# Kernel optimization log

Hardware: AMD Instinct MI355X
Metric: run time of the kernel (lower is better)

The kernel has to match this reference:

```python
import jax, jax.numpy as jnp
import numpy as np

DIM = 2048
HEADS = 16
HEAD_DIM = DIM // HEADS
B, S = 2, 2048


def setup_inputs() -> dict:
    key = jax.random.key(0)
    k1, k2, k3 = jax.random.split(key, 3)
    x = jax.random.normal(k1, (B, S, DIM), dtype=jnp.float32)
    # causal mask (True = keep), realistic production usage of masked_fill(mask==0,...)
    mask = jnp.tril(jnp.ones((S, S), dtype=bool))
    scale = 1.0 / np.sqrt(DIM)
    W_qkv = jax.random.normal(k2, (DIM, 3 * DIM), dtype=jnp.float32) * scale
    b_qkv = jnp.zeros((3 * DIM,), dtype=jnp.float32)
    W_out = jax.random.normal(k3, (DIM, DIM), dtype=jnp.float32) * scale
    b_out = jnp.zeros((DIM,), dtype=jnp.float32)
    return {"x": x, "mask": mask, "W_qkv": W_qkv, "b_qkv": b_qkv,
            "W_out": W_out, "b_out": b_out}


def reference(x, mask, W_qkv, b_qkv, W_out, b_out):
    b, s, d = x.shape
    # fused QKV projection: [b,s,3d]
    qkv = jnp.einsum('bsd,de->bse', x, W_qkv) + b_qkv
    # [b, s, h, 3*hd] -> [b, h, s, 3*hd] -> chunk into q,k,v
    qkv = qkv.reshape(b, s, HEADS, 3 * HEAD_DIM).transpose(0, 2, 1, 3)
    q, k, v = jnp.split(qkv, 3, axis=-1)  # each [b,h,s,hd]
    scores = jnp.einsum('bhqd,bhkd->bhqk', q, k) / np.sqrt(HEAD_DIM)
    scores = jnp.where(mask, scores, jnp.float32(-1e9))
    attn = jax.nn.softmax(scores, axis=-1)
    # dropout_rate = 0.0 (eval) -> identity
    out = jnp.einsum('bhqk,bhkd->bhqd', attn, v)  # [b,h,s,hd]
    out = out.transpose(0, 2, 1, 3).reshape(b, s, d)
    return jnp.einsum('bsd,de->bse', out, W_out) + b_out
```

## Files before the change

kernel.cpp:

```cpp
#include <hip/hip_runtime.h>
#include <hip/hip_bf16.h>

#define SEQ   2048
#define DIMSZ 2048
#define NHEAD 16
#define HD    128
#define KDIM  2048

typedef __attribute__((ext_vector_type(8))) short bf16x8;
typedef __attribute__((ext_vector_type(4))) float f32x4;
typedef __attribute__((ext_vector_type(4))) short short4v;
typedef __attribute__((ext_vector_type(4))) float float4v;

__device__ __forceinline__ short f2bf(float f) {
    union { __hip_bfloat16 h; short s; } u;
    u.h = __float2bfloat16(f);
    return u.s;
}

__device__ __forceinline__ void gload_lds16(const void* g, void* l) {
    __builtin_amdgcn_global_load_lds(
        (const __attribute__((address_space(1))) void*)g,
        (__attribute__((address_space(3))) void*)l, 16, 0, 0);
}

__global__ __launch_bounds__(256) void cvt_bf16(const float* __restrict__ in,
                                                short* __restrict__ out) {
    int i = (blockIdx.x * 256 + threadIdx.x) * 4;
    float4v v = *reinterpret_cast<const float4v*>(in + i);
    short4v o;
    o[0] = f2bf(v[0]); o[1] = f2bf(v[1]); o[2] = f2bf(v[2]); o[3] = f2bf(v[3]);
    *reinterpret_cast<short4v*>(out + i) = o;
}

__global__ __launch_bounds__(256) void transpose_cvt(const float* __restrict__ in,
                                                     short* __restrict__ out,
                                                     int R, int C) {
    __shared__ float tile[32][33];
    int c0 = blockIdx.x * 32, r0 = blockIdx.y * 32;
    int tx = threadIdx.x, ty = threadIdx.y;
#pragma unroll
    for (int i = 0; i < 32; i += 8)
        tile[ty + i][tx] = in[(long)(r0 + ty + i) * C + c0 + tx];
    __syncthreads();
#pragma unroll
    for (int i = 0; i < 32; i += 8)
        out[(long)(c0 + ty + i) * R + r0 + tx] = f2bf(tile[tx][ty + i]);
}

template <int MODE>
__global__ __launch_bounds__(256) void gemm_bt(const short* __restrict__ A,
                                               const short* __restrict__ Bt,
                                               const float* __restrict__ bias,
                                               float* __restrict__ outf,
                                               short* __restrict__ q_buf,
                                               short* __restrict__ k_buf,
                                               short* __restrict__ vt_buf) {
    __shared__ short Alds[128 * 64];
    __shared__ short Blds[128 * 64];
    const int tid = threadIdx.x;
    const int wave = tid >> 6, lane = tid & 63;
    const int lr = lane & 15, lg = lane >> 4;
    const int m0 = blockIdx.y * 128, n0 = blockIdx.x * 128;
    const int wr = (wave >> 1) * 64, wc = (wave & 1) * 64;
    const short* Ab = A + (long)m0 * KDIM;
    const short* Bb = Bt + (long)n0 * KDIM;
    const int srow = tid >> 3;
    const int sch = (tid & 7) * 8;

    f32x4 acc[4][4] = {};

    for (int kt = 0; kt < KDIM; kt += 64) {
#pragma unroll
        for (int i = 0; i < 4; ++i) {
            gload_lds16(Ab + (long)(i * 32 + srow) * KDIM + kt + sch,
                        &Alds[(i * 256 + wave * 64) * 8]);
            gload_lds16(Bb + (long)(i * 32 + srow) * KDIM + kt + sch,
                        &Blds[(i * 256 + wave * 64) * 8]);
        }
        __syncthreads();
#pragma unroll
        for (int kk = 0; kk < 2; ++kk) {
            bf16x8 af[4], bfr[4];
#pragma unroll
            for (int mi = 0; mi < 4; ++mi)
                af[mi] = *reinterpret_cast<const bf16x8*>(
                    &Alds[(wr + mi * 16 + lr) * 64 + kk * 32 + lg * 8]);
#pragma unroll
            for (int ni = 0; ni < 4; ++ni)
                bfr[ni] = *reinterpret_cast<const bf16x8*>(
                    &Blds[(wc + ni * 16 + lr) * 64 + kk * 32 + lg * 8]);
#pragma unroll
            for (int mi = 0; mi < 4; ++mi)
#pragma unroll
                for (int ni = 0; ni < 4; ++ni)
                    acc[mi][ni] = __builtin_amdgcn_mfma_f32_16x16x32_bf16(
                        af[mi], bfr[ni], acc[mi][ni], 0, 0, 0);
        }
        __syncthreads();
    }

#pragma unroll
    for (int mi = 0; mi < 4; ++mi) {
#pragma unroll
        for (int ni = 0; ni < 4; ++ni) {
            int col = n0 + wc + ni * 16 + lr;
            float bv = bias[col];
#pragma unroll
            for (int j = 0; j < 4; ++j) {
                int row = m0 + wr + mi * 16 + lg * 4 + j;
                float v = acc[mi][ni][j] + bv;
                if (MODE == 0) {
                    int h = col / (3 * HD);
                    int jj = col - h * (3 * HD);
                    int b = row >> 11, s = row & 2047;
                    int bh = b * NHEAD + h;
                    short sv = f2bf(v);
                    if (jj < HD)
                        q_buf[(bh * SEQ + s) * HD + jj] = sv;
                    else if (jj < 2 * HD)
                        k_buf[(bh * SEQ + s) * HD + (jj - HD)] = sv;
                    else
                        vt_buf[(bh * HD + (jj - 2 * HD)) * SEQ + s] = sv;
                } else {
                    outf[(long)row * DIMSZ + col] = v;
                }
            }
        }
    }
}

__global__ __launch_bounds__(256, 2) void attn_kernel(const short* __restrict__ q_buf,
                                                      const short* __restrict__ k_buf,
                                                      const short* __restrict__ vt_buf,
                                                      short* __restrict__ ao) {
    __shared__ __align__(16) short Klds[2][64 * 128];
    __shared__ __align__(16) short Vlds[2][128 * 64];
    __shared__ __align__(16) short Plds[4][32 * 64];
    const int tid = threadIdx.x;
    const int wave = tid >> 6, lane = tid & 63;
    const int lr = lane & 15, lg = lane >> 4;
    const int bx = blockIdx.x;
    const int qt = 15 - (bx >> 5);
    const int bh = bx & 31;
    const int b = bh >> 4, h = bh & 15;
    const int qbase = qt * 128 + wave * 32;
    const float scale = 0.08838834764831845f;

    bf16x8 qf[2][4];
    {
        const short* qrow = q_buf + ((long)(bh * SEQ + qbase + lr)) * HD;
#pragma unroll
        for (int mi = 0; mi < 2; ++mi)
#pragma unroll
            for (int c = 0; c < 4; ++c)
                qf[mi][c] = *reinterpret_cast<const bf16x8*>(
                    qrow + mi * 16 * HD + c * 32 + lg * 8);
    }
    asm volatile("s_waitcnt vmcnt(0)" ::: "memory");

    const char* kbase = (const char*)(k_buf + (long)bh * SEQ * HD);
    const char* vbase = (const char*)(vt_buf + (long)bh * HD * SEQ);
    const int krow_l = wave * 4 + (lane >> 4);
    const int kcol_l = ((lane & 15) * 16) ^ ((krow_l & 7) << 4);
    const int vrow_l = wave * 8 + (lane >> 3);
    const int vcol_l = ((lane & 7) * 16) ^ ((vrow_l & 7) << 4);

    const int nt = 2 * (qt + 1);
    auto stage = [&](int bufi, int t) {
        const char* ks = kbase + (long)t * 16384 + (long)krow_l * 256 + kcol_l;
        const char* vs = vbase + (long)t * 128 + (long)vrow_l * (SEQ * 2) + vcol_l;
        short* kd = &Klds[bufi][wave * 512];
        short* vd = &Vlds[bufi][wave * 512];
#pragma unroll
        for (int i = 0; i < 4; ++i) {
            gload_lds16(ks + i * 4096, kd + i * 2048);
            gload_lds16(vs + (long)i * 32 * SEQ * 2, vd + i * 2048);
        }
    };

    f32x4 o_acc[2][8] = {};
    float mrow[2][4], lrow[2][4];
#pragma unroll
    for (int mi = 0; mi < 2; ++mi)
#pragma unroll
        for (int j = 0; j < 4; ++j) { mrow[mi][j] = -1e30f; lrow[mi][j] = 0.f; }
    short* pw = &Plds[wave][0];

    stage(0, 0);
    for (int t = 0; t < nt; ++t) {
        const int cur = t & 1;
        if (t + 1 < nt) {
            stage(cur ^ 1, t + 1);
            asm volatile("s_waitcnt vmcnt(8)" ::: "memory");
        } else {
            asm volatile("s_waitcnt vmcnt(0)" ::: "memory");
        }
        __builtin_amdgcn_s_barrier();
        __builtin_amdgcn_sched_barrier(0);

        const int kv0 = t * 64;
        if (kv0 <= qbase + 31) {
            f32x4 sc[2][4] = {};
            const short* kl = &Klds[cur][0];
#pragma unroll
            for (int c = 0; c < 4; ++c) {
                bf16x8 kf[4];
#pragma unroll
                for (int ni = 0; ni < 4; ++ni)
                    kf[ni] = *reinterpret_cast<const bf16x8*>(
                        kl + (((ni * 16 + lr) * 256 +
                               ((c * 64 + lg * 16) ^ ((lr & 7) << 4))) >> 1));
#pragma unroll
                for (int mi = 0; mi < 2; ++mi)
#pragma unroll
                    for (int ni = 0; ni < 4; ++ni)
                        sc[mi][ni] = __builtin_amdgcn_mfma_f32_16x16x32_bf16(
                            qf[mi][c], kf[ni], sc[mi][ni], 0, 0, 0);
            }
            const bool full = (kv0 + 63) <= qbase;
            float pv[2][4][4], pm[2][4];
#pragma unroll
            for (int mi = 0; mi < 2; ++mi)
#pragma unroll
                for (int j = 0; j < 4; ++j) {
                    float mx = -3e38f;
#pragma unroll
                    for (int ni = 0; ni < 4; ++ni) {
                        float v = sc[mi][ni][j] * scale;
                        if (!full) {
                            int qg = qbase + mi * 16 + lg * 4 + j;
                            if (kv0 + ni * 16 + lr > qg) v = -1e9f;
                        }
                        pv[mi][ni][j] = v;
                        mx = fmaxf(mx, v);
                    }
                    pm[mi][j] = mx;
                }
#pragma unroll
            for (int m = 1; m < 16; m <<= 1)
#pragma unroll
                for (int mi = 0; mi < 2; ++mi)
#pragma unroll
                    for (int j = 0; j < 4; ++j)
                        pm[mi][j] = fmaxf(pm[mi][j], __shfl_xor(pm[mi][j], m, 64));
            float alpha[2][4], psum[2][4];
#pragma unroll
            for (int mi = 0; mi < 2; ++mi)
#pragma unroll
                for (int j = 0; j < 4; ++j) {
                    float mn = fmaxf(mrow[mi][j], pm[mi][j]);
                    alpha[mi][j] = __expf(mrow[mi][j] - mn);
                    mrow[mi][j] = mn;
                    psum[mi][j] = 0.f;
                }
#pragma unroll
            for (int mi = 0; mi < 2; ++mi)
#pragma unroll
                for (int ni = 0; ni < 4; ++ni)
#pragma unroll
                    for (int j = 0; j < 4; ++j) {
                        float p = __expf(pv[mi][ni][j] - mrow[mi][j]);
                        pv[mi][ni][j] = p;
                        psum[mi][j] += p;
                    }
#pragma unroll
            for (int m = 1; m < 16; m <<= 1)
#pragma unroll
                for (int mi = 0; mi < 2; ++mi)
#pragma unroll
                    for (int j = 0; j < 4; ++j)
                        psum[mi][j] += __shfl_xor(psum[mi][j], m, 64);
#pragma unroll
            for (int mi = 0; mi < 2; ++mi)
#pragma unroll
                for (int j = 0; j < 4; ++j)
                    lrow[mi][j] = lrow[mi][j] * alpha[mi][j] + psum[mi][j];
#pragma unroll
            for (int mi = 0; mi < 2; ++mi)
#pragma unroll
                for (int n = 0; n < 8; ++n)
#pragma unroll
                    for (int j = 0; j < 4; ++j)
                        o_acc[mi][n][j] *= alpha[mi][j];
#pragma unroll
            for (int mi = 0; mi < 2; ++mi)
#pragma unroll
                for (int ni = 0; ni < 4; ++ni)
#pragma unroll
                    for (int j = 0; j < 4; ++j) {
                        int row = mi * 16 + lg * 4 + j;
                        int cb = (ni * 32 + lr * 2) ^ ((row & 7) << 4);
                        pw[(row * 128 + cb) >> 1] = f2bf(pv[mi][ni][j]);
                    }
            const short* vl = &Vlds[cur][0];
#pragma unroll
            for (int kc = 0; kc < 2; ++kc) {
                bf16x8 pa[2];
#pragma unroll
                for (int mi = 0; mi < 2; ++mi)
                    pa[mi] = *reinterpret_cast<const bf16x8*>(
                        pw + (((mi * 16 + lr) * 128 +
                               ((kc * 64 + lg * 16) ^ ((lr & 7) << 4))) >> 1));
#pragma unroll
                for (int n = 0; n < 8; ++n) {
                    bf16x8 vf = *reinterpret_cast<const bf16x8*>(
                        vl + (((n * 16 + lr) * 128 +
                               ((kc * 64 + lg * 16) ^ ((lr & 7) << 4))) >> 1));
#pragma unroll
                    for (int mi = 0; mi < 2; ++mi)
                        o_acc[mi][n] = __builtin_amdgcn_mfma_f32_16x16x32_bf16(
                            pa[mi], vf, o_acc[mi][n], 0, 0, 0);
                }
            }
        }
        __builtin_amdgcn_s_barrier();
    }

    float inv[2][4];
#pragma unroll
    for (int mi = 0; mi < 2; ++mi)
#pragma unroll
        for (int j = 0; j < 4; ++j) inv[mi][j] = 1.0f / lrow[mi][j];
    short* aor = ao + ((long)(b * SEQ + qbase) * DIMSZ + h * HD);
#pragma unroll
    for (int mi = 0; mi < 2; ++mi)
#pragma unroll
        for (int n = 0; n < 8; ++n)
#pragma unroll
            for (int j = 0; j < 4; ++j)
                aor[(mi * 16 + lg * 4 + j) * DIMSZ + n * 16 + lr] =
                    f2bf(o_acc[mi][n][j] * inv[mi][j]);
}

extern "C" void kernel_launch(void* const* d_in, const int* in_sizes, int n_in,
                              void* d_out, int out_size, void* d_ws, size_t ws_size,
                              hipStream_t stream) {
    const float* x     = (const float*)d_in[0];
    const float* W_qkv = (const float*)d_in[2];
    const float* b_qkv = (const float*)d_in[3];
    const float* W_out = (const float*)d_in[4];
    const float* b_out = (const float*)d_in[5];
    float* out = (float*)d_out;

    char* ws = (char*)d_ws;
    short* x_bf   = (short*)ws;
    short* wqkv_t = (short*)(ws + (size_t)16 * 1048576);
    short* wout_t = (short*)(ws + (size_t)40 * 1048576);
    short* q_buf  = (short*)(ws + (size_t)48 * 1048576);
    short* k_buf  = (short*)(ws + (size_t)64 * 1048576);
    short* vt_buf = (short*)(ws + (size_t)80 * 1048576);
    short* ao     = x_bf;

    cvt_bf16<<<8192, 256, 0, stream>>>(x, x_bf);
    transpose_cvt<<<dim3(192, 64), dim3(32, 8), 0, stream>>>(W_qkv, wqkv_t, 2048, 6144);
    transpose_cvt<<<dim3(64, 64), dim3(32, 8), 0, stream>>>(W_out, wout_t, 2048, 2048);
    gemm_bt<0><<<dim3(48, 32), 256, 0, stream>>>(x_bf, wqkv_t, b_qkv, nullptr,
                                                 q_buf, k_buf, vt_buf);
    attn_kernel<<<512, 256, 0, stream>>>(q_buf, k_buf, vt_buf, ao);
    gemm_bt<1><<<dim3(16, 32), 256, 0, stream>>>(ao, wout_t, b_out, out,
                                                 nullptr, nullptr, nullptr);
}
```

Baseline: 339.9 us.

## Replace GEMM with 256x256 8-wave double-buffered pipelined kernel with LDS swizzle

New measurement: 352.3 us. 3.6% more time.

```diff
diff --git a/kernel.cpp b/kernel.cpp
--- a/kernel.cpp
+++ b/kernel.cpp
@@ -49,81 +49,191 @@
 }
 
 template <int MODE>
-__global__ __launch_bounds__(256) void gemm_bt(const short* __restrict__ A,
-                                               const short* __restrict__ Bt,
-                                               const float* __restrict__ bias,
-                                               float* __restrict__ outf,
-                                               short* __restrict__ q_buf,
-                                               short* __restrict__ k_buf,
-                                               short* __restrict__ vt_buf) {
-    __shared__ short Alds[128 * 64];
-    __shared__ short Blds[128 * 64];
+__global__ __launch_bounds__(512, 2) void gemm8p(const short* __restrict__ A,
+                                                 const short* __restrict__ Bt,
+                                                 const float* __restrict__ bias,
+                                                 float* __restrict__ outf,
+                                                 short* __restrict__ q_buf,
+                                                 short* __restrict__ k_buf,
+                                                 short* __restrict__ vt_buf,
+                                                 int ntx) {
+    __shared__ __align__(16) short Alds[2][256 * 64];
+    __shared__ __align__(16) short Blds[2][256 * 64];
     const int tid = threadIdx.x;
-    const int wave = tid >> 6, lane = tid & 63;
-    const int lr = lane & 15, lg = lane >> 4;
-    const int m0 = blockIdx.y * 128, n0 = blockIdx.x * 128;
-    const int wr = (wave >> 1) * 64, wc = (wave & 1) * 64;
-    const short* Ab = A + (long)m0 * KDIM;
-    const short* Bb = Bt + (long)n0 * KDIM;
-    const int srow = tid >> 3;
-    const int sch = (tid & 7) * 8;
-
-    f32x4 acc[4][4] = {};
-
-    for (int kt = 0; kt < KDIM; kt += 64) {
-#pragma unroll
-        for (int i = 0; i < 4; ++i) {
-            gload_lds16(Ab + (long)(i * 32 + srow) * KDIM + kt + sch,
-                        &Alds[(i * 256 + wave * 64) * 8]);
-            gload_lds16(Bb + (long)(i * 32 + srow) * KDIM + kt + sch,
-                        &Blds[(i * 256 + wave * 64) * 8]);
-        }
-        __syncthreads();
-#pragma unroll
-        for (int kk = 0; kk < 2; ++kk) {
-            bf16x8 af[4], bfr[4];
+    const int wv = tid >> 6, ln = tid & 63;
+    const int lr = ln & 15, lg = ln >> 4;
+    const int wr = wv >> 2, wc = wv & 3;
+    const int q8 = gridDim.x >> 3;
+    const int id = blockIdx.x;
+    const int swz = (id & 7) * q8 + (id >> 3);
+    const int m0 = (swz / ntx) * 256, n0 = (swz % ntx) * 256;
+
+    const int r_l = wv * 8 + (ln >> 3);
+    const int g8 = ((ln & 7) ^ ((ln >> 3) & 7)) << 3;
+
+    auto stA = [&](int bufi, int half, int T) {
+#pragma unroll
+        for (int i = 0; i < 2; ++i)
+            gload_lds16(A + (long)(m0 + half * 128 + i * 64 + r_l) * KDIM + T * 64 + g8,
+                        &Alds[bufi][half * 8192 + i * 4096 + wv * 512]);
+    };
+    auto stB = [&](int bufi, int half, int T) {
+#pragma unroll
+        for (int i = 0; i < 2; ++i)
+            gload_lds16(Bt + (long)(n0 + half * 128 + i * 64 + r_l) * KDIM + T * 64 + g8,
+                        &Blds[bufi][half * 8192 + i * 4096 + wv * 512]);
+    };
+
+    f32x4 acc[4][4][2] = {};
+
+    stA(0, 0, 0); stB(0, 0, 0); stA(0, 1, 0); stB(0, 1, 0);
+    stA(1, 0, 1); stB(1, 0, 1);
+    asm volatile("s_waitcnt vmcnt(4)" ::: "memory");
+    __builtin_amdgcn_s_barrier();
+    __builtin_amdgcn_sched_barrier(0);
+
+    const int NT = KDIM / 64;
+    int cur = 0;
+    for (int T = 0; T < NT; ++T, cur ^= 1) {
+        const short* Al = &Alds[cur][0];
+        const short* Bl = &Blds[cur][0];
+        auto rdA = [&](int r, int kk) {
+            return *reinterpret_cast<const bf16x8*>(
+                &Al[r * 64 + (((kk * 4 + lg) ^ (r & 7)) << 3)]);
+        };
+        auto rdB = [&](int r, int kk) {
+            return *reinterpret_cast<const bf16x8*>(
+                &Bl[r * 64 + (((kk * 4 + lg) ^ (r & 7)) << 3)]);
+        };
+        bf16x8 af[4][2], bf[2][2];
+
+#pragma unroll
+        for (int mi = 0; mi < 4; ++mi) {
+            af[mi][0] = rdA(wr * 64 + mi * 16 + lr, 0);
+            af[mi][1] = rdA(wr * 64 + mi * 16 + lr, 1);
+        }
+#pragma unroll
+        for (int ni = 0; ni < 2; ++ni) {
+            bf[ni][0] = rdB(wc * 32 + ni * 16 + lr, 0);
+            bf[ni][1] = rdB(wc * 32 + ni * 16 + lr, 1);
+        }
+        if (T + 1 < NT) stA(cur ^ 1, 1, T + 1);
+        __builtin_amdgcn_s_barrier();
+        __builtin_amdgcn_sched_barrier(0);
+        __builtin_amdgcn_s_setprio(1);
+#pragma unroll
+        for (int kk = 0; kk < 2; ++kk)
 #pragma unroll
             for (int mi = 0; mi < 4; ++mi)
-                af[mi] = *reinterpret_cast<const bf16x8*>(
-                    &Alds[(wr + mi * 16 + lr) * 64 + kk * 32 + lg * 8]);
-#pragma unroll
-            for (int ni = 0; ni < 4; ++ni)
-                bfr[ni] = *reinterpret_cast<const bf16x8*>(
-                    &Blds[(wc + ni * 16 + lr) * 64 + kk * 32 + lg * 8]);
+#pragma unroll
+                for (int ni = 0; ni < 2; ++ni)
+                    acc[0][mi][ni] = __builtin_amdgcn_mfma_f32_16x16x32_bf16(
+                        af[mi][kk], bf[ni][kk], acc[0][mi][ni], 0, 0, 0);
+        __builtin_amdgcn_s_setprio(0);
+        __builtin_amdgcn_s_barrier();
+        __builtin_amdgcn_sched_barrier(0);
+
+#pragma unroll
+        for (int ni = 0; ni < 2; ++ni) {
+            bf[ni][0] = rdB(128 + wc * 32 + ni * 16 + lr, 0);
+            bf[ni][1] = rdB(128 + wc * 32 + ni * 16 + lr, 1);
+        }
+        if (T + 1 < NT) stB(cur ^ 1, 1, T + 1);
+        __builtin_amdgcn_s_barrier();
+        __builtin_amdgcn_sched_barrier(0);
+        __builtin_amdgcn_s_setprio(1);
+#pragma unroll
+        for (int kk = 0; kk < 2; ++kk)
 #pragma unroll
             for (int mi = 0; mi < 4; ++mi)
 #pragma unroll
-                for (int ni = 0; ni < 4; ++ni)
-                    acc[mi][ni] = __builtin_amdgcn_mfma_f32_16x16x32_bf16(
-                        af[mi], bfr[ni], acc[mi][ni], 0, 0, 0);
-        }
-        __syncthreads();
+                for (int ni = 0; ni < 2; ++ni)
+                    acc[1][mi][ni] = __builtin_amdgcn_mfma_f32_16x16x32_bf16(
+                        af[mi][kk], bf[ni][kk], acc[1][mi][ni], 0, 0, 0);
+        __builtin_amdgcn_s_setprio(0);
+        __builtin_amdgcn_s_barrier();
+        __builtin_amdgcn_sched_barrier(0);
+
+#pragma unroll
+        for (int mi = 0; mi < 4; ++mi) {
+            af[mi][0] = rdA(128 + wr * 64 + mi * 16 + lr, 0);
+            af[mi][1] = rdA(128 + wr * 64 + mi * 16 + lr, 1);
+        }
+#pragma unroll
+        for (int ni = 0; ni < 2; ++ni) {
+            bf[ni][0] = rdB(wc * 32 + ni * 16 + lr, 0);
+            bf[ni][1] = rdB(wc * 32 + ni * 16 + lr, 1);
+        }
+        if (T + 2 < NT) stA(cur, 0, T + 2);
+        __builtin_amdgcn_s_barrier();
+        __builtin_amdgcn_sched_barrier(0);
+        __builtin_amdgcn_s_setprio(1);
+#pragma unroll
+        for (int kk = 0; kk < 2; ++kk)
+#pragma unroll
+            for (int mi = 0; mi < 4; ++mi)
+#pragma unroll
+                for (int ni = 0; ni < 2; ++ni)
+                    acc[2][mi][ni] = __builtin_amdgcn_mfma_f32_16x16x32_bf16(
+                        af[mi][kk], bf[ni][kk], acc[2][mi][ni], 0, 0, 0);
+        __builtin_amdgcn_s_setprio(0);
+        __builtin_amdgcn_s_barrier();
+        __builtin_amdgcn_sched_barrier(0);
+
+#pragma unroll
+        for (int ni = 0; ni < 2; ++ni) {
+            bf[ni][0] = rdB(128 + wc * 32 + ni * 16 + lr, 0);
+            bf[ni][1] = rdB(128 + wc * 32 + ni * 16 + lr, 1);
+        }
+        if (T + 2 < NT) stB(cur, 0, T + 2);
+        __builtin_amdgcn_s_barrier();
+        __builtin_amdgcn_sched_barrier(0);
+        __builtin_amdgcn_s_setprio(1);
+#pragma unroll
+        for (int kk = 0; kk < 2; ++kk)
+#pragma unroll
+            for (int mi = 0; mi < 4; ++mi)
+#pragma unroll
+                for (int ni = 0; ni < 2; ++ni)
+                    acc[3][mi][ni] = __builtin_amdgcn_mfma_f32_16x16x32_bf16(
+                        af[mi][kk], bf[ni][kk], acc[3][mi][ni], 0, 0, 0);
+        __builtin_amdgcn_s_setprio(0);
+        if (T + 2 < NT)
+            asm volatile("s_waitcnt vmcnt(4)" ::: "memory");
+        else if (T + 1 < NT)
+            asm volatile("s_waitcnt vmcnt(0)" ::: "memory");
+        __builtin_amdgcn_s_barrier();
+        __builtin_amdgcn_sched_barrier(0);
     }
 
 #pragma unroll
-    for (int mi = 0; mi < 4; ++mi) {
-#pragma unroll
-        for (int ni = 0; ni < 4; ++ni) {
-            int col = n0 + wc + ni * 16 + lr;
-            float bv = bias[col];
-#pragma unroll
-            for (int j = 0; j < 4; ++j) {
-                int row = m0 + wr + mi * 16 + lg * 4 + j;
-                float v = acc[mi][ni][j] + bv;
-                if (MODE == 0) {
-                    int h = col / (3 * HD);
-                    int jj = col - h * (3 * HD);
-                    int b = row >> 11, s = row & 2047;
-                    int bh = b * NHEAD + h;
-                    short sv = f2bf(v);
-                    if (jj < HD)
-                        q_buf[(bh * SEQ + s) * HD + jj] = sv;
-                    else if (jj < 2 * HD)
-                        k_buf[(bh * SEQ + s) * HD + (jj - HD)] = sv;
-                    else
-                        vt_buf[(bh * HD + (jj - 2 * HD)) * SEQ + s] = sv;
-                } else {
-                    outf[(long)row * DIMSZ + col] = v;
+    for (int q = 0; q < 4; ++q) {
+        const int mh = q >> 1, nh = q & 1;
+#pragma unroll
+        for (int mi = 0; mi < 4; ++mi) {
+#pragma unroll
+            for (int ni = 0; ni < 2; ++ni) {
+                int col = n0 + nh * 128 + wc * 32 + ni * 16 + lr;
+                float bv = bias[col];
+#pragma unroll
+                for (int j = 0; j < 4; ++j) {
+                    int row = m0 + mh * 128 + wr * 64 + mi * 16 + lg * 4 + j;
+                    float v = acc[q][mi][ni][j] + bv;
+                    if (MODE == 0) {
+                        int h = col / (3 * HD);
+                        int jj = col - h * (3 * HD);
+                        int b = row >> 11, s = row & 2047;
+                        int bh = b * NHEAD + h;
+                        short sv = f2bf(v);
+                        if (jj < HD)
+                            q_buf[(bh * SEQ + s) * HD + jj] = sv;
+                        else if (jj < 2 * HD)
+                            k_buf[(bh * SEQ + s) * HD + (jj - HD)] = sv;
+                        else
+                            vt_buf[(bh * HD + (jj - 2 * HD)) * SEQ + s] = sv;
+                    } else {
+                        outf[(long)row * DIMSZ + col] = v;
+                    }
                 }
             }
         }
@@ -355,9 +465,9 @@
     cvt_bf16<<<8192, 256, 0, stream>>>(x, x_bf);
     transpose_cvt<<<dim3(192, 64), dim3(32, 8), 0, stream>>>(W_qkv, wqkv_t, 2048, 6144);
     transpose_cvt<<<dim3(64, 64), dim3(32, 8), 0, stream>>>(W_out, wout_t, 2048, 2048);
-    gemm_bt<0><<<dim3(48, 32), 256, 0, stream>>>(x_bf, wqkv_t, b_qkv, nullptr,
-                                                 q_buf, k_buf, vt_buf);
+    gemm8p<0><<<384, 512, 0, stream>>>(x_bf, wqkv_t, b_qkv, nullptr,
+                                       q_buf, k_buf, vt_buf, 24);
     attn_kernel<<<512, 256, 0, stream>>>(q_buf, k_buf, vt_buf, ao);
-    gemm_bt<1><<<dim3(16, 32), 256, 0, stream>>>(ao, wout_t, b_out, out,
-                                                 nullptr, nullptr, nullptr);
-}
+    gemm8p<1><<<128, 512, 0, stream>>>(ao, wout_t, b_out, out,
+                                       nullptr, nullptr, nullptr, 8);
+}
```

## Replace GEMM with 8-wave double-buffered ping-pong pipelined kernel

Applied to the files above, without the earlier changes.

Result: faster. 327.8 us (-3.6%).

```diff
diff --git a/kernel.cpp b/kernel.cpp
--- a/kernel.cpp
+++ b/kernel.cpp
@@ -48,86 +48,194 @@
         out[(long)(c0 + ty + i) * R + r0 + tx] = f2bf(tile[tx][ty + i]);
 }
 
-template <int MODE>
-__global__ __launch_bounds__(256) void gemm_bt(const short* __restrict__ A,
-                                               const short* __restrict__ Bt,
-                                               const float* __restrict__ bias,
-                                               float* __restrict__ outf,
-                                               short* __restrict__ q_buf,
-                                               short* __restrict__ k_buf,
-                                               short* __restrict__ vt_buf) {
-    __shared__ short Alds[128 * 64];
-    __shared__ short Blds[128 * 64];
+template <int MODE, int BM, int BN, int WMC, int WNC>
+__global__ __launch_bounds__(512, 2) void gemm8p(const short* __restrict__ A,
+                                                 const short* __restrict__ Bt,
+                                                 const float* __restrict__ bias,
+                                                 float* __restrict__ outf,
+                                                 short* __restrict__ q_buf,
+                                                 short* __restrict__ k_buf,
+                                                 short* __restrict__ vt_buf,
+                                                 int ntx) {
+    constexpr int QMW = (BM / 2) / WMC;
+    constexpr int QNW = (BN / 2) / WNC;
+    constexpr int MA = QMW / 16;
+    constexpr int NB = QNW / 16;
+    constexpr int UA = BM / 64, UB = BN / 64, UT = UA + UB;
+    constexpr int RA = MA * 2, RB = NB * 2;
+    constexpr int BH0C = (BN / 2 + 63) / 64;
+    constexpr int NE = UA / 2 + BH0C, NL = UT - NE;
+    constexpr int S0 = 2, S2 = 2;
+    constexpr int VM0 = NE + S0;
+    constexpr int VM2 = NL + S2;
+    constexpr int VM3 = (NE - S2) + NE;
+    constexpr int NT = KDIM / 64;
+
+    __shared__ __align__(16) short Alds[2][BM * 64];
+    __shared__ __align__(16) short Blds[2][BN * 64];
+
     const int tid = threadIdx.x;
-    const int wave = tid >> 6, lane = tid & 63;
-    const int lr = lane & 15, lg = lane >> 4;
-    const int m0 = blockIdx.y * 128, n0 = blockIdx.x * 128;
-    const int wr = (wave >> 1) * 64, wc = (wave & 1) * 64;
-    const short* Ab = A + (long)m0 * KDIM;
-    const short* Bb = Bt + (long)n0 * KDIM;
-    const int srow = tid >> 3;
-    const int sch = (tid & 7) * 8;
-
-    f32x4 acc[4][4] = {};
-
-    for (int kt = 0; kt < KDIM; kt += 64) {
-#pragma unroll
-        for (int i = 0; i < 4; ++i) {
-            gload_lds16(Ab + (long)(i * 32 + srow) * KDIM + kt + sch,
-                        &Alds[(i * 256 + wave * 64) * 8]);
-            gload_lds16(Bb + (long)(i * 32 + srow) * KDIM + kt + sch,
-                        &Blds[(i * 256 + wave * 64) * 8]);
-        }
-        __syncthreads();
-#pragma unroll
-        for (int kk = 0; kk < 2; ++kk) {
-            bf16x8 af[4], bfr[4];
-#pragma unroll
-            for (int mi = 0; mi < 4; ++mi)
-                af[mi] = *reinterpret_cast<const bf16x8*>(
-                    &Alds[(wr + mi * 16 + lr) * 64 + kk * 32 + lg * 8]);
-#pragma unroll
-            for (int ni = 0; ni < 4; ++ni)
-                bfr[ni] = *reinterpret_cast<const bf16x8*>(
-                    &Blds[(wc + ni * 16 + lr) * 64 + kk * 32 + lg * 8]);
-#pragma unroll
-            for (int mi = 0; mi < 4; ++mi)
-#pragma unroll
-                for (int ni = 0; ni < 4; ++ni)
-                    acc[mi][ni] = __builtin_amdgcn_mfma_f32_16x16x32_bf16(
-                        af[mi], bfr[ni], acc[mi][ni], 0, 0, 0);
-        }
-        __syncthreads();
-    }
-
-#pragma unroll
-    for (int mi = 0; mi < 4; ++mi) {
-#pragma unroll
-        for (int ni = 0; ni < 4; ++ni) {
-            int col = n0 + wc + ni * 16 + lr;
-            float bv = bias[col];
-#pragma unroll
-            for (int j = 0; j < 4; ++j) {
-                int row = m0 + wr + mi * 16 + lg * 4 + j;
-                float v = acc[mi][ni][j] + bv;
-                if (MODE == 0) {
-                    int h = col / (3 * HD);
-                    int jj = col - h * (3 * HD);
-                    int b = row >> 11, s = row & 2047;
-                    int bh = b * NHEAD + h;
-                    short sv = f2bf(v);
-                    if (jj < HD)
-                        q_buf[(bh * SEQ + s) * HD + jj] = sv;
-                    else if (jj < 2 * HD)
-                        k_buf[(bh * SEQ + s) * HD + (jj - HD)] = sv;
-                    else
-                        vt_buf[(bh * HD + (jj - 2 * HD)) * SEQ + s] = sv;
-                } else {
-                    outf[(long)row * DIMSZ + col] = v;
+    const int wv = tid >> 6, ln = tid & 63;
+    const int lr = ln & 15, lg = ln >> 4;
+    const int wm = wv / WNC, wn = wv % WNC;
+    const int q8 = gridDim.x >> 3;
+    const int id = blockIdx.x;
+    const int swz = (id & 7) * q8 + (id >> 3);
+    const int m0 = (swz / ntx) * BM, n0 = (swz % ntx) * BN;
+
+    const int r_l = wv * 8 + (ln >> 3);
+    const int g8 = ((ln & 7) ^ ((ln >> 3) & 7)) << 3;
+
+#define STAGE_U(u, bufi, TT)                                                   \
+    {                                                                          \
+        const bool isA_ = (u) < UA / 2 || (u) >= UA / 2 + UB;                  \
+        const int idx_ = (u) < UA / 2 ? (u)                                    \
+                         : ((u) < UA / 2 + UB ? (u) - UA / 2 : (u) - UB);      \
+        if (isA_)                                                              \
+            gload_lds16(A + (long)(m0 + idx_ * 64 + r_l) * KDIM + (TT)*64 + g8,\
+                        &Alds[bufi][idx_ * 4096 + wv * 512]);                  \
+        else                                                                   \
+            gload_lds16(Bt + (long)(n0 + idx_ * 64 + r_l) * KDIM + (TT)*64 + g8,\
+                        &Blds[bufi][idx_ * 4096 + wv * 512]);                  \
+    }
+
+#define RD(L_, row_, kk_) \
+    (*reinterpret_cast<const bf16x8*>(&(L_)[(row_)*64 + ((((kk_)*4 + lg) ^ ((row_)&7)) << 3)]))
+
+#define RD_A(bufi, mh, bank)                                                   \
+    _Pragma("unroll") for (int mi = 0; mi < MA; ++mi) {                        \
+        int r_ = (mh) * (BM / 2) + wm * QMW + mi * 16 + lr;                    \
+        bank[mi][0] = RD(Alds[bufi], r_, 0);                                   \
+        bank[mi][1] = RD(Alds[bufi], r_, 1);                                   \
+    }
+#define RD_B(bufi, nh, bank)                                                   \
+    _Pragma("unroll") for (int ni = 0; ni < NB; ++ni) {                        \
+        int r_ = (nh) * (BN / 2) + wn * QNW + ni * 16 + lr;                    \
+        bank[ni][0] = RD(Blds[bufi], r_, 0);                                   \
+        bank[ni][1] = RD(Blds[bufi], r_, 1);                                   \
+    }
+
+#define MFMA_Q(qi, AB, BB)                                                     \
+    __builtin_amdgcn_s_setprio(1);                                             \
+    _Pragma("unroll") for (int kk = 0; kk < 2; ++kk)                           \
+        _Pragma("unroll") for (int mi = 0; mi < MA; ++mi)                      \
+            _Pragma("unroll") for (int ni = 0; ni < NB; ++ni)                  \
+                acc[qi][mi][ni] = __builtin_amdgcn_mfma_f32_16x16x32_bf16(     \
+                    AB[mi][kk], BB[ni][kk], acc[qi][mi][ni], 0, 0, 0);         \
+    __builtin_amdgcn_s_setprio(0);
+
+#define LGKM(n)                                                                \
+    asm volatile("s_waitcnt lgkmcnt(%0)" ::"i"(n) : "memory");                 \
+    __builtin_amdgcn_sched_barrier(0);
+#define VMC(n) asm volatile("s_waitcnt vmcnt(%0)" ::"i"(n) : "memory");
+#define BAR()                                                                  \
+    __builtin_amdgcn_s_barrier();                                              \
+    __builtin_amdgcn_sched_barrier(0);
+
+    f32x4 acc[4][MA][NB] = {};
+    bf16x8 aF0[MA][2], aF1[MA][2], bF0a[NB][2], bF0b[NB][2], bF1[NB][2];
+
+#pragma unroll
+    for (int u = 0; u < UT; ++u) STAGE_U(u, 0, 0);
+#pragma unroll
+    for (int u = 0; u < NE; ++u) STAGE_U(u, 1, 1);
+    VMC(NE);
+    BAR();
+    RD_A(0, 0, aF0);
+    RD_B(0, 0, bF0a);
+
+#define TILE_BODY(PAR, T_, BF0C, BF0N)                                         \
+    {                                                                          \
+        constexpr int cur = PAR, nxt = PAR ^ 1;                                \
+                 \
+        RD_B(cur, 1, bF1);                                                     \
+        if ((T_) + 1 < NT) {                                                   \
+            STAGE_U(NE + 0, nxt, (T_) + 1);                                    \
+            STAGE_U(NE + 1, nxt, (T_) + 1);                                    \
+        }                                                                      \
+        LGKM(RB);                                                              \
+        MFMA_Q(0, aF0, BF0C);                                                  \
+        VMC(VM0);                                                              \
+        BAR();                                                                 \
+                \
+        RD_A(cur, 1, aF1);                                                     \
+        if ((T_) + 1 < NT) {                                                   \
+            _Pragma("unroll") for (int u = NE + S0; u < UT; ++u)               \
+                STAGE_U(u, nxt, (T_) + 1);                                     \
+        }                                                                      \
+        LGKM(RA);                                                              \
+        MFMA_Q(1, aF0, bF1);                                                   \
+        BAR();                                                                 \
+                       \
+        if ((T_) + 2 < NT) {                                                   \
+            STAGE_U(0, cur, (T_) + 2);                                         \
+            STAGE_U(1, cur, (T_) + 2);                                         \
+        }                                                                      \
+        LGKM(0);                                                               \
+        MFMA_Q(2, aF1, bF1);                                                   \
+        if ((T_) + 2 < NT) { VMC(VM2); } else { VMC(NL); }                     \
+        BAR();                                                                 \
+           \
+        if ((T_) + 1 < NT) {                                                   \
+            RD_A(nxt, 0, aF0);                                                 \
+            RD_B(nxt, 0, BF0N);                                                \
+        }                                                                      \
+        if ((T_) + 2 < NT) {                                                   \
+            _Pragma("unroll") for (int u = S2; u < NE; ++u)                    \
+                STAGE_U(u, cur, (T_) + 2);                                     \
+        }                                                                      \
+        LGKM(RA + RB);                                                         \
+        MFMA_Q(3, aF1, BF0C);                                                  \
+        if ((T_) + 2 < NT) { VMC(VM3); } else { VMC(0); }                      \
+        BAR();                                                                 \
+    }
+
+    for (int TT = 0; TT < NT; TT += 2) {
+        TILE_BODY(0, TT, bF0a, bF0b);
+        TILE_BODY(1, TT + 1, bF0b, bF0a);
+    }
+
+    const int MH[4] = {0, 0, 1, 1}, NHq[4] = {0, 1, 1, 0};
+#pragma unroll
+    for (int q = 0; q < 4; ++q) {
+#pragma unroll
+        for (int mi = 0; mi < MA; ++mi) {
+#pragma unroll
+            for (int ni = 0; ni < NB; ++ni) {
+                int col = n0 + NHq[q] * (BN / 2) + wn * QNW + ni * 16 + lr;
+                float bv = bias[col];
+#pragma unroll
+                for (int j = 0; j < 4; ++j) {
+                    int row = m0 + MH[q] * (BM / 2) + wm * QMW + mi * 16 + lg * 4 + j;
+                    float v = acc[q][mi][ni][j] + bv;
+                    if (MODE == 0) {
+                        int h = col / (3 * HD);
+                        int jj = col - h * (3 * HD);
+                        int b = row >> 11, s = row & 2047;
+                        int bh = b * NHEAD + h;
+                        short sv = f2bf(v);
+                        if (jj < HD)
+                            q_buf[(bh * SEQ + s) * HD + jj] = sv;
+                        else if (jj < 2 * HD)
+                            k_buf[(bh * SEQ + s) * HD + (jj - HD)] = sv;
+                        else
+                            vt_buf[(bh * HD + (jj - 2 * HD)) * SEQ + s] = sv;
+                    } else {
+                        outf[(long)row * DIMSZ + col] = v;
+                    }
                 }
             }
         }
     }
+#undef STAGE_U
+#undef RD
+#undef RD_A
+#undef RD_B
+#undef MFMA_Q
+#undef LGKM
+#undef VMC
+#undef BAR
+#undef TILE_BODY
 }
 
 __global__ __launch_bounds__(256, 2) void attn_kernel(const short* __restrict__ q_buf,
@@ -355,9 +463,9 @@
     cvt_bf16<<<8192, 256, 0, stream>>>(x, x_bf);
     transpose_cvt<<<dim3(192, 64), dim3(32, 8), 0, stream>>>(W_qkv, wqkv_t, 2048, 6144);
     transpose_cvt<<<dim3(64, 64), dim3(32, 8), 0, stream>>>(W_out, wout_t, 2048, 2048);
-    gemm_bt<0><<<dim3(48, 32), 256, 0, stream>>>(x_bf, wqkv_t, b_qkv, nullptr,
-                                                 q_buf, k_buf, vt_buf);
+    gemm8p<0, 256, 192, 4, 2><<<512, 512, 0, stream>>>(x_bf, wqkv_t, b_qkv, nullptr,
+                                                       q_buf, k_buf, vt_buf, 32);
     attn_kernel<<<512, 256, 0, stream>>>(q_buf, k_buf, vt_buf, ao);
-    gemm_bt<1><<<dim3(16, 32), 256, 0, stream>>>(ao, wout_t, b_out, out,
-                                                 nullptr, nullptr, nullptr);
-}
+    gemm8p<1, 128, 256, 2, 4><<<256, 512, 0, stream>>>(ao, wout_t, b_out, out,
+                                                       nullptr, nullptr, nullptr, 8);
+}
```
